# Kernel tuning notes

Hardware: AMD Instinct MI355X
Metric: run time of the kernel (lower is better)

## Reference

```python
import jax, jax.numpy as jnp
import numpy as np

B, R, S, T, F = 16, 4, 4, 14, 2048  # batch, rx ants, streams, ofdm symbols, subcarriers


def setup_inputs() -> dict:
    key = jax.random.key(0)
    ks = jax.random.split(key, 5)
    y_re = jax.random.normal(ks[0], (B, R, T, F), jnp.float32)
    y_im = jax.random.normal(ks[1], (B, R, T, F), jnp.float32)
    h_re = jax.random.normal(ks[2], (B, R, S, T, F), jnp.float32)
    h_im = jax.random.normal(ks[3], (B, R, S, T, F), jnp.float32)
    mask = jax.random.randint(ks[4], (T, F), 0, 2, jnp.int32)  # MU_MIMO_RG_populated
    noise_var = jnp.array([0.1], jnp.float32)
    return {"y_re": y_re, "y_im": y_im, "h_re": h_re, "h_im": h_im,
            "mask": mask, "noise_var": noise_var}


def _sic_lmmse(y, h, no):
    # y: [B,T,F,R] complex, h: [B,T,F,R,S] complex, no: scalar noise variance
    eyeS = jnp.eye(S, dtype=jnp.complex64)
    y_res = y
    xs, ns = [], []
    for k in range(S):  # fixed detection order over the 4 streams
        m = (jnp.arange(S) >= k).astype(jnp.complex64)  # remaining (undetected) streams
        Hm = h * m  # zero out already-cancelled stream columns
        gram0 = jnp.einsum('...rs,...rt->...st', jnp.conj(Hm), Hm)  # [.,S,S] Hm^H Hm
        A = gram0 + no * eyeS                                        # LMMSE matrix
        Ainv = jnp.linalg.inv(A)                                     # batched 4x4 inverse
        z = jnp.einsum('...rs,...r->...s', jnp.conj(Hm), y_res)     # Hm^H y_res
        xz = jnp.einsum('...st,...t->...s', Ainv, z)                 # unbiased-unscaled estimate
        d = jnp.einsum('...t,...t->...', Ainv[..., k, :], gram0[..., :, k])  # (Ainv gram0)_kk
        xk = xz[..., k] / d                                          # bias-corrected LMMSE estimate
        ne = jnp.real((1.0 - d) / d)                                 # effective post-eq noise var
        y_res = y_res - h[..., :, k] * xk[..., None]                 # soft interference cancellation
        xs.append(xk)
        ns.append(ne)
    x_hat = jnp.stack(xs, -1)   # [B,T,F,S]
    no_eff = jnp.stack(ns, -1)  # [B,T,F,S]
    return x_hat, no_eff


def reference(y_re, y_im, h_re, h_im, mask, noise_var):
    y = jax.lax.complex(y_re, y_im)             # [B,R,T,F]
    h = jax.lax.complex(h_re, h_im)             # [B,R,S,T,F]
    y = jnp.transpose(y, (0, 2, 3, 1))          # [B,T,F,R]
    h = jnp.transpose(h, (0, 3, 4, 1, 2))       # [B,T,F,R,S]
    no = noise_var[0]
    x_hat, no_eff = _sic_lmmse(y, h, no)
    m = mask.astype(jnp.float32)[None, :, :, None]  # populated-RE mask [1,T,F,1]
    x_hat = x_hat * m
    no_eff = no_eff * m
    x_hat = jnp.transpose(x_hat, (0, 3, 1, 2))   # [B,S,T,F]
    no_eff = jnp.transpose(no_eff, (0, 3, 1, 2))
    x_ri = jnp.stack([jnp.real(x_hat), jnp.imag(x_hat)], 0)  # [2,B,S,T,F] real view
    return x_ri, no_eff
```

## Files before the change

### kernel.cpp

```cpp
#include <hip/hip_runtime.h>

#define B_ 16
#define R_ 4
#define S_ 4
#define T_ 14
#define F_ 2048
constexpr int P_ = F_ / 2;

typedef float vf __attribute__((ext_vector_type(2)));

struct cplx { vf re, im; };

__device__ __forceinline__ vf vsp(float s){ vf r; r.x = s; r.y = s; return r; }
__device__ __forceinline__ vf vrcp(vf x){ vf r; r.x = __builtin_amdgcn_rcpf(x.x); r.y = __builtin_amdgcn_rcpf(x.y); return r; }
__device__ __forceinline__ vf vrsq(vf x){ vf r; r.x = __builtin_amdgcn_rsqf(x.x); r.y = __builtin_amdgcn_rsqf(x.y); return r; }

__device__ __forceinline__ cplx cmul(cplx a, cplx b) {
    return {a.re*b.re - a.im*b.im, a.re*b.im + a.im*b.re};
}
__device__ __forceinline__ cplx cmulc(cplx a, cplx b) {
    return {a.re*b.re + a.im*b.im, a.re*b.im - a.im*b.re};
}
__device__ __forceinline__ cplx cadd(cplx a, cplx b){ return {a.re+b.re, a.im+b.im}; }
__device__ __forceinline__ cplx csub(cplx a, cplx b){ return {a.re-b.re, a.im-b.im}; }
__device__ __forceinline__ cplx cscale(cplx a, vf s){ return {a.re*s, a.im*s}; }
__device__ __forceinline__ cplx conjc(cplx a){ return {a.re, -a.im}; }

__global__ __launch_bounds__(256) void sic_lmmse_kernel(
    const float* __restrict__ y_re_, const float* __restrict__ y_im_,
    const float* __restrict__ h_re_, const float* __restrict__ h_im_,
    const int* __restrict__ mask, const float* __restrict__ nv,
    float* __restrict__ out_)
{
    constexpr int N    = B_ * T_ * P_;
    constexpr int BSTP = B_ * S_ * T_ * P_;

    int idx = blockIdx.x * 256 + threadIdx.x;
    int fv = idx % P_;
    int bt = idx / P_;
    int t  = bt % T_;
    int b  = bt / T_;

    const vf* y_re = (const vf*)y_re_;
    const vf* y_im = (const vf*)y_im_;
    const vf* h_re = (const vf*)h_re_;
    const vf* h_im = (const vf*)h_im_;
    vf*       out  = (vf*)out_;

    float no  = nv[0];
    vf    vno = vsp(no);

    int2 mi = ((const int2*)mask)[t * P_ + fv];
    vf m; m.x = (float)mi.x; m.y = (float)mi.y;

    cplx g[4][4];
    cplx z[4];
    #pragma unroll
    for (int i = 0; i < 4; i++) {
        z[i] = { vsp(0.f), vsp(0.f) };
        #pragma unroll
        for (int j = 0; j <= i; j++) g[i][j] = { vsp(0.f), vsp(0.f) };
    }

    #pragma unroll
    for (int r = 0; r < 4; r++) {
        int ybase = ((b * R_ + r) * T_ + t) * P_ + fv;
        cplx yr = { y_re[ybase], y_im[ybase] };
        cplx hr[4];
        #pragma unroll
        for (int s = 0; s < 4; s++) {
            int hbase = (((b * R_ + r) * S_ + s) * T_ + t) * P_ + fv;
            hr[s] = { h_re[hbase], h_im[hbase] };
        }
        #pragma unroll
        for (int s = 0; s < 4; s++) {
            z[s] = cadd(z[s], cmulc(hr[s], yr));
            #pragma unroll
            for (int u = 0; u <= s; u++)
                g[s][u] = cadd(g[s][u], cmulc(hr[s], hr[u]));
        }
    }

    cplx Lm[4][4];
    vf dinv[4];
    #pragma unroll
    for (int i = 0; i < 4; i++) {
        #pragma unroll
        for (int j = 0; j < i; j++) {
            cplx s = g[i][j];
            #pragma unroll
            for (int p = 0; p < j; p++)
                s = csub(s, cmul(Lm[i][p], conjc(Lm[j][p])));
            Lm[i][j] = cscale(s, dinv[j]);
        }
        vf dd = g[i][i].re + vno;
        #pragma unroll
        for (int p = 0; p < i; p++)
            dd = dd - (Lm[i][p].re * Lm[i][p].re + Lm[i][p].im * Lm[i][p].im);
        dinv[i] = vrsq(dd);
    }

    cplx M[4][4];
    #pragma unroll
    for (int i = 0; i < 4; i++) {
        #pragma unroll
        for (int j = 0; j < i; j++) {
            cplx s = { vsp(0.f), vsp(0.f) };
            #pragma unroll
            for (int p = j; p < i; p++)
                s = cadd(s, cmul(Lm[i][p], M[p][j]));
            M[i][j] = cscale(s, -dinv[i]);
        }
        M[i][i] = { dinv[i], vsp(0.f) };
    }

    cplx W[4][4];
    #pragma unroll
    for (int i = 0; i < 4; i++) {
        #pragma unroll
        for (int j = 0; j <= i; j++) {
            cplx s = { vsp(0.f), vsp(0.f) };
            #pragma unroll
            for (int p = i; p < 4; p++)
                s = cadd(s, cmul(conjc(M[p][i]), M[p][j]));
            W[i][j] = s;
        }
    }

    cplx zc[4];
    #pragma unroll
    for (int j = 0; j < 4; j++) zc[j] = z[j];

    #pragma unroll
    for (int k = 0; k < 4; k++) {
        const int n = 4 - k;
        vf e = W[0][0].re;
        cplx xz = cscale(zc[0], e);
        #pragma unroll
        for (int j = 1; j < 4; j++) {
            if (j < n) xz = cadd(xz, cmul(conjc(W[j][0]), zc[j]));
        }
        vf d    = vsp(1.0f) - vno * e;
        vf drcp = vrcp(d);
        cplx xk = cscale(xz, drcp);
        vf ne   = vno * e * drcp;

        int obase = ((b * S_ + k) * T_ + t) * P_ + fv;
        out[obase]            = xk.re * m;
        out[BSTP + obase]     = xk.im * m;
        out[2 * BSTP + obase] = ne * m;

        if (k < 3) {
            vf einv = vrcp(e);
            #pragma unroll
            for (int j = 1; j < 4; j++) {
                if (j < n) zc[j - 1] = csub(zc[j], cmul(g[k + j][k], xk));
            }
            cplx W2[3][3];
            #pragma unroll
            for (int i = 1; i < 4; i++) {
                #pragma unroll
                for (int j = 1; j <= i; j++) {
                    if (i < n)
                        W2[i - 1][j - 1] =
                            csub(W[i][j], cscale(cmul(W[i][0], conjc(W[j][0])), einv));
                }
            }
            #pragma unroll
            for (int i = 0; i < 3; i++) {
                #pragma unroll
                for (int j = 0; j <= i; j++) {
                    if (i < n - 1) W[i][j] = W2[i][j];
                }
            }
        }
    }
}

extern "C" void kernel_launch(void* const* d_in, const int* in_sizes, int n_in,
                              void* d_out, int out_size, void* d_ws, size_t ws_size,
                              hipStream_t stream) {
    const float* y_re = (const float*)d_in[0];
    const float* y_im = (const float*)d_in[1];
    const float* h_re = (const float*)d_in[2];
    const float* h_im = (const float*)d_in[3];
    const int*   mask = (const int*)  d_in[4];
    const float* nv   = (const float*)d_in[5];
    float* out = (float*)d_out;

    constexpr int N = B_ * T_ * P_;
    int threads = 256;
    int blocks  = N / threads;
    hipLaunchKernelGGL(sic_lmmse_kernel, dim3(blocks), dim3(threads), 0, stream,
                       y_re, y_im, h_re, h_im, mask, nv, out);
}
```

Before: 111.7 us.

## Replace Cholesky-inverse plus Schur downdates with reverse-order UL factorization

Replaces the forward Cholesky, the triangular inverse, the explicit W=M^H M product and the per-stage Schur-complement downdates with a single reverse-order (UL) Cholesky factorization. In that factorization the leading diagonal entries directly give each stage's inverse diagonal, and the rows of the inverted triangular factor give the filter for each stage. The Gram diagonal is also kept real-only. This cuts ALU work and register pressure in a kernel that is largely memory bound, at the cost of a fully hand-unrolled, harder-to-verify formulation.

```diff
diff --git a/kernel.cpp b/kernel.cpp
--- a/kernel.cpp
+++ b/kernel.cpp
@@ -21,10 +21,14 @@
 __device__ __forceinline__ cplx cmulc(cplx a, cplx b) {
     return {a.re*b.re + a.im*b.im, a.re*b.im - a.im*b.re};
 }
+__device__ __forceinline__ cplx cmulcb(cplx a, cplx b) {
+    return {a.re*b.re + a.im*b.im, a.im*b.re - a.re*b.im};
+}
 __device__ __forceinline__ cplx cadd(cplx a, cplx b){ return {a.re+b.re, a.im+b.im}; }
 __device__ __forceinline__ cplx csub(cplx a, cplx b){ return {a.re-b.re, a.im-b.im}; }
 __device__ __forceinline__ cplx cscale(cplx a, vf s){ return {a.re*s, a.im*s}; }
 __device__ __forceinline__ cplx conjc(cplx a){ return {a.re, -a.im}; }
+__device__ __forceinline__ vf cnorm(cplx a){ return a.re*a.re + a.im*a.im; }
 
 __global__ __launch_bounds__(256) void sic_lmmse_kernel(
     const float* __restrict__ y_re_, const float* __restrict__ y_im_,
@@ -32,7 +36,6 @@
     const int* __restrict__ mask, const float* __restrict__ nv,
     float* __restrict__ out_)
 {
-    constexpr int N    = B_ * T_ * P_;
     constexpr int BSTP = B_ * S_ * T_ * P_;
 
     int idx = blockIdx.x * 256 + threadIdx.x;
@@ -53,14 +56,13 @@
     int2 mi = ((const int2*)mask)[t * P_ + fv];
     vf m; m.x = (float)mi.x; m.y = (float)mi.y;
 
-    cplx g[4][4];
+    cplx g10, g20, g30, g21, g31, g32;
+    vf   g00, g11, g22, g33;
     cplx z[4];
     #pragma unroll
-    for (int i = 0; i < 4; i++) {
-        z[i] = { vsp(0.f), vsp(0.f) };
-        #pragma unroll
-        for (int j = 0; j <= i; j++) g[i][j] = { vsp(0.f), vsp(0.f) };
-    }
+    for (int i = 0; i < 4; i++) z[i] = { vsp(0.f), vsp(0.f) };
+    g10 = g20 = g30 = g21 = g31 = g32 = { vsp(0.f), vsp(0.f) };
+    g00 = g11 = g22 = g33 = vsp(0.f);
 
     #pragma unroll
     for (int r = 0; r < 4; r++) {
@@ -73,107 +75,92 @@
             hr[s] = { h_re[hbase], h_im[hbase] };
         }
         #pragma unroll
-        for (int s = 0; s < 4; s++) {
-            z[s] = cadd(z[s], cmulc(hr[s], yr));
-            #pragma unroll
-            for (int u = 0; u <= s; u++)
-                g[s][u] = cadd(g[s][u], cmulc(hr[s], hr[u]));
-        }
+        for (int s = 0; s < 4; s++) z[s] = cadd(z[s], cmulc(hr[s], yr));
+        g00 = g00 + cnorm(hr[0]);
+        g11 = g11 + cnorm(hr[1]);
+        g22 = g22 + cnorm(hr[2]);
+        g33 = g33 + cnorm(hr[3]);
+        g10 = cadd(g10, cmulc(hr[1], hr[0]));
+        g20 = cadd(g20, cmulc(hr[2], hr[0]));
+        g30 = cadd(g30, cmulc(hr[3], hr[0]));
+        g21 = cadd(g21, cmulc(hr[2], hr[1]));
+        g31 = cadd(g31, cmulc(hr[3], hr[1]));
+        g32 = cadd(g32, cmulc(hr[3], hr[2]));
     }
 
-    cplx Lm[4][4];
-    vf dinv[4];
-    #pragma unroll
-    for (int i = 0; i < 4; i++) {
-        #pragma unroll
-        for (int j = 0; j < i; j++) {
-            cplx s = g[i][j];
-            #pragma unroll
-            for (int p = 0; p < j; p++)
-                s = csub(s, cmul(Lm[i][p], conjc(Lm[j][p])));
-            Lm[i][j] = cscale(s, dinv[j]);
-        }
-        vf dd = g[i][i].re + vno;
-        #pragma unroll
-        for (int p = 0; p < i; p++)
-            dd = dd - (Lm[i][p].re * Lm[i][p].re + Lm[i][p].im * Lm[i][p].im);
-        dinv[i] = vrsq(dd);
+    vf r3 = vrsq(g33 + vno);
+    cplx U03 = cscale(conjc(g30), r3);
+    cplx U13 = cscale(conjc(g31), r3);
+    cplx U23 = cscale(conjc(g32), r3);
+
+    vf r2 = vrsq(g22 + vno - cnorm(U23));
+    cplx U02 = cscale(csub(conjc(g20), cmulcb(U03, U23)), r2);
+    cplx U12 = cscale(csub(conjc(g21), cmulcb(U13, U23)), r2);
+
+    vf r1 = vrsq(g11 + vno - cnorm(U12) - cnorm(U13));
+    cplx U01 = cscale(csub(csub(conjc(g10), cmulcb(U02, U12)), cmulcb(U03, U13)), r1);
+
+    vf r0 = vrsq(g00 + vno - cnorm(U01) - cnorm(U02) - cnorm(U03));
+
+    cplx V01 = cscale(cscale(U01, r1), -r0);
+    cplx V12 = cscale(cscale(U12, r2), -r1);
+    cplx V23 = cscale(cscale(U23, r3), -r2);
+    cplx V02 = cscale(cadd(cmul(U01, V12), cscale(U02, r2)), -r0);
+    cplx V13 = cscale(cadd(cmul(U12, V23), cscale(U13, r3)), -r1);
+    cplx V03 = cscale(cadd(cadd(cmul(U01, V13), cmul(U02, V23)), cscale(U03, r3)), -r0);
+
+    int obase0 = ((b * S_) * T_ + t) * P_ + fv;
+    constexpr int OSTRIDE = T_ * P_;
+
+    {
+        cplx ts = cadd(cadd(cscale(z[0], r0), cmul(V01, z[1])),
+                       cadd(cmul(V02, z[2]), cmul(V03, z[3])));
+        vf e = r0 * r0;
+        vf drcp = vrcp(vsp(1.0f) - vno * e);
+        cplx xk = cscale(ts, r0 * drcp);
+        vf ne = vno * e * drcp;
+        out[obase0]            = xk.re * m;
+        out[BSTP + obase0]     = xk.im * m;
+        out[2*BSTP + obase0]   = ne * m;
+        z[0] = csub(z[1], cmul(g10, xk));
+        z[1] = csub(z[2], cmul(g20, xk));
+        z[2] = csub(z[3], cmul(g30, xk));
     }
-
-    cplx M[4][4];
-    #pragma unroll
-    for (int i = 0; i < 4; i++) {
-        #pragma unroll
-        for (int j = 0; j < i; j++) {
-            cplx s = { vsp(0.f), vsp(0.f) };
-            #pragma unroll
-            for (int p = j; p < i; p++)
-                s = cadd(s, cmul(Lm[i][p], M[p][j]));
-            M[i][j] = cscale(s, -dinv[i]);
-        }
-        M[i][i] = { dinv[i], vsp(0.f) };
+    {
+        cplx ts = cadd(cadd(cscale(z[0], r1), cmul(V12, z[1])), cmul(V13, z[2]));
+        vf e = r1 * r1;
+        vf drcp = vrcp(vsp(1.0f) - vno * e);
+        cplx xk = cscale(ts, r1 * drcp);
+        vf ne = vno * e * drcp;
+        int ob = obase0 + OSTRIDE;
+        out[ob]            = xk.re * m;
+        out[BSTP + ob]     = xk.im * m;
+        out[2*BSTP + ob]   = ne * m;
+        z[0] = csub(z[1], cmul(g21, xk));
+        z[1] = csub(z[2], cmul(g31, xk));
     }
-
-    cplx W[4][4];
-    #pragma unroll
-    for (int i = 0; i < 4; i++) {
-        #pragma unroll
-        for (int j = 0; j <= i; j++) {
-            cplx s = { vsp(0.f), vsp(0.f) };
-            #pragma unroll
-            for (int p = i; p < 4; p++)
-                s = cadd(s, cmul(conjc(M[p][i]), M[p][j]));
-            W[i][j] = s;
-        }
+    {
+        cplx ts = cadd(cscale(z[0], r2), cmul(V23, z[1]));
+        vf e = r2 * r2;
+        vf drcp = vrcp(vsp(1.0f) - vno * e);
+        cplx xk = cscale(ts, r2 * drcp);
+        vf ne = vno * e * drcp;
+        int ob = obase0 + 2 * OSTRIDE;
+        out[ob]            = xk.re * m;
+        out[BSTP + ob]     = xk.im * m;
+        out[2*BSTP + ob]   = ne * m;
+        z[0] = csub(z[1], cmul(g32, xk));
     }
-
-    cplx zc[4];
-    #pragma unroll
-    for (int j = 0; j < 4; j++) zc[j] = z[j];
-
-    #pragma unroll
-    for (int k = 0; k < 4; k++) {
-        const int n = 4 - k;
-        vf e = W[0][0].re;
-        cplx xz = cscale(zc[0], e);
-        #pragma unroll
-        for (int j = 1; j < 4; j++) {
-            if (j < n) xz = cadd(xz, cmul(conjc(W[j][0]), zc[j]));
-        }
-        vf d    = vsp(1.0f) - vno * e;
-        vf drcp = vrcp(d);
-        cplx xk = cscale(xz, drcp);
-        vf ne   = vno * e * drcp;
-
-        int obase = ((b * S_ + k) * T_ + t) * P_ + fv;
-        out[obase]            = xk.re * m;
-        out[BSTP + obase]     = xk.im * m;
-        out[2 * BSTP + obase] = ne * m;
-
-        if (k < 3) {
-            vf einv = vrcp(e);
-            #pragma unroll
-            for (int j = 1; j < 4; j++) {
-                if (j < n) zc[j - 1] = csub(zc[j], cmul(g[k + j][k], xk));
-            }
-            cplx W2[3][3];
-            #pragma unroll
-            for (int i = 1; i < 4; i++) {
-                #pragma unroll
-                for (int j = 1; j <= i; j++) {
-                    if (i < n)
-                        W2[i - 1][j - 1] =
-                            csub(W[i][j], cscale(cmul(W[i][0], conjc(W[j][0])), einv));
-                }
-            }
-            #pragma unroll
-            for (int i = 0; i < 3; i++) {
-                #pragma unroll
-                for (int j = 0; j <= i; j++) {
-                    if (i < n - 1) W[i][j] = W2[i][j];
-                }
-            }
-        }
+    {
+        cplx ts = cscale(z[0], r3);
+        vf e = r3 * r3;
+        vf drcp = vrcp(vsp(1.0f) - vno * e);
+        cplx xk = cscale(ts, r3 * drcp);
+        vf ne = vno * e * drcp;
+        int ob = obase0 + 3 * OSTRIDE;
+        out[ob]            = xk.re * m;
+        out[BSTP + ob]     = xk.im * m;
+        out[2*BSTP + ob]   = ne * m;
     }
 }
 
```

Measured after the change: 113.6 us. Within noise of the previous version (+1.7%).
